# Kernel tuning notes

Hardware: AMD Instinct MI355X
Metric: run time of the kernel (lower is better)

Reference implementation:

```python
import jax, jax.numpy as jnp
import numpy as np


def setup_inputs() -> dict:
    key = jax.random.key(0)
    k1, k2, k3, k4 = jax.random.split(key, 4)
    batch, T, state_dim, action_dim = 64, 1024, 512, 128
    x0 = jax.random.normal(k1, (batch, state_dim), dtype=jnp.float32)
    us = jax.random.normal(k2, (batch, T, action_dim), dtype=jnp.float32)
    # Scale A so the 1024-step linear recurrence stays bounded (spectral radius < 1)
    A = jax.random.normal(k3, (state_dim, state_dim), dtype=jnp.float32) * (0.9 / np.sqrt(state_dim))
    B = jax.random.normal(k4, (action_dim, state_dim), dtype=jnp.float32) * (1.0 / np.sqrt(action_dim))
    return {"x0": x0, "us": us, "A": A, "B": B}


def reference(x0, us, A, B):
    """Linear SSM rollout: x_{t+1} = x_t @ A + u_t @ B, returns xs [batch, T, state_dim]."""
    us_t = jnp.swapaxes(us, 0, 1)  # [T, batch, action_dim]

    def step(x, u):
        x_next = x @ A + u @ B  # [batch, state_dim]
        return x_next, x_next

    _, xs = jax.lax.scan(step, x0, us_t)  # xs: [T, batch, state_dim]
    return jnp.swapaxes(xs, 0, 1)  # [batch, T, state_dim]
```

## Files before the change

### kernel.cpp

```cpp
#include <hip/hip_runtime.h>


typedef __attribute__((ext_vector_type(8))) short bf16x8;
typedef __attribute__((ext_vector_type(8))) unsigned short ushort8;
typedef __attribute__((ext_vector_type(4))) float f32x4;
typedef unsigned short ushort_t;

#define MFMA16(a, b, c) __builtin_amdgcn_mfma_f32_16x16x32_bf16(a, b, c, 0, 0, 0)

#define OFF_AT  0UL
#define OFF_AU  8912896UL
#define OFF_BT  15204352UL
#define OFF_BU  15335424UL
#define OFF_WT  15466496UL
#define OFF_Z   16515072UL
#define OFF_E1S 41680896UL
#define OFF_E2S 50069504UL

__host__ __device__ __forceinline__ int slot_of(int p) {
    if (p == 0) return 16;
    if (p <= 8) return p - 1;
    return 7 + (p >> 3);
}

__device__ __forceinline__ unsigned short f2bf(float f) {
    union { float f; unsigned u; } v; v.f = f;
    unsigned r = v.u + 0x7FFFu + ((v.u >> 16) & 1u);
    return (unsigned short)(r >> 16);
}

__device__ __forceinline__ int sel4(int4 v, int p) {
    return p == 0 ? v.x : p == 1 ? v.y : p == 2 ? v.z : v.w;
}

typedef __attribute__((address_space(3))) unsigned int as3_u32;
typedef __attribute__((address_space(1))) const unsigned int as1_u32;
__device__ __forceinline__ void gll16(const void* g, void* l) {
    __builtin_amdgcn_global_load_lds((as1_u32*)g, (as3_u32*)l, 16, 0, 0);
}

__global__ __launch_bounds__(256) void prep_kernel(const float* __restrict__ x0,
                                                   const float* __restrict__ us,
                                                   const float* __restrict__ A,
                                                   const float* __restrict__ B,
                                                   char* __restrict__ ws) {
    ushort_t* At1 = (ushort_t*)(ws + OFF_AT);
    ushort_t* Au1 = (ushort_t*)(ws + OFF_AU);
    ushort_t* Bt  = (ushort_t*)(ws + OFF_BT);
    ushort_t* Bu  = (ushort_t*)(ws + OFF_BU);
    ushort_t* X0b = (ushort_t*)(ws + OFF_E2S);
    ushort_t* Z   = (ushort_t*)(ws + OFF_Z);
    long idx = (long)blockIdx.x * 256 + threadIdx.x;
    if (idx < 262144) {
        Au1[idx] = f2bf(A[idx]);
    } else if (idx < 524288) {
        long gi = idx - 262144;
        int n = (int)(gi >> 9), k = (int)(gi & 511);
        At1[gi] = f2bf(A[(long)k * 512 + n]);
    } else if (idx < 589824) {
        long i2 = idx - 524288;
        int kp = (int)(i2 >> 9), n = (int)(i2 & 511);
        ushort_t v = f2bf(B[i2]);
        Bt[(long)n * 128 + kp] = v;
        Bu[i2] = v;
    } else if (idx < 593920) {
        long gi = idx - 589824;
        long e0 = gi * 8;
        float4 v0 = *(const float4*)(x0 + e0);
        float4 v1 = *(const float4*)(x0 + e0 + 4);
        ushort8 h = { f2bf(v0.x), f2bf(v0.y), f2bf(v0.z), f2bf(v0.w),
                      f2bf(v1.x), f2bf(v1.y), f2bf(v1.z), f2bf(v1.w) };
        *(ushort8*)(X0b + e0) = h;
    } else if (idx < 1642496) {
        long gi = idx - 593920;
        int row = (int)(gi >> 7), g8 = (int)(gi & 127);
        int c = row >> 6, b = row & 63;
        const float* src = us + (long)b * 131072 + c * 1024 + g8 * 8;
        float4 v0 = *(const float4*)src;
        float4 v1 = *(const float4*)(src + 4);
        ushort8 h = { f2bf(v0.x), f2bf(v0.y), f2bf(v0.z), f2bf(v0.w),
                      f2bf(v1.x), f2bf(v1.y), f2bf(v1.z), f2bf(v1.w) };
        *(ushort8*)(Z + (long)row * 1536 + 512 + g8 * 8) = h;
    } else {
        long gi2 = idx - 1642496;
        if (gi2 < 262144) {
            int n = (int)(gi2 >> 9), k2 = (int)(gi2 & 511);
            At1[(long)16 * 262144 + gi2] = (n == k2) ? (ushort_t)0x3F80 : (ushort_t)0;
        }
    }
}

__global__ __launch_bounds__(256) void pow_stage(char* __restrict__ ws,
                                                 int4 dd, int4 mm, int4 ii, int dual) {
    __shared__ ushort_t ldsX[64 * 512];
    ushort_t* At = (ushort_t*)(ws + OFF_AT);
    ushort_t* Au = (ushort_t*)(ws + OFF_AU);

    int bx = blockIdx.x;
    int nb = bx & 3, mb = (bx >> 2) & 7;
    int prod, pair;
    if (dual) { prod = (bx >> 5) & 1; pair = bx >> 6; }
    else      { prod = 0;             pair = bx >> 5; }
    int d = sel4(dd, pair), m_ = sel4(mm, pair), i_ = sel4(ii, pair);

    const ushort_t *Xp, *Yp; ushort_t* outp;
    if (prod == 0) { Xp = At + (long)slot_of(m_) * 262144; Yp = Au + (long)slot_of(i_) * 262144; outp = At + (long)slot_of(d) * 262144; }
    else           { Xp = Au + (long)slot_of(i_) * 262144; Yp = At + (long)slot_of(m_) * 262144; outp = Au + (long)slot_of(d) * 262144; }

    int tid = threadIdx.x, w = tid >> 6, lane = tid & 63, q = lane >> 4, r = lane & 15;

    for (int i2 = tid; i2 < 64 * 64; i2 += 256) {
        int row = i2 >> 6, c8 = i2 & 63;
        ushort8 v = *(const ushort8*)(Xp + (long)(mb * 64 + row) * 512 + c8 * 8);
        *(ushort8*)&ldsX[row * 512 + ((c8 ^ (row & 7)) << 3)] = v;
    }
    __syncthreads();

    f32x4 acc[4][2];
    for (int a1 = 0; a1 < 4; a1++) for (int b1 = 0; b1 < 2; b1++) acc[a1][b1] = (f32x4){0.f, 0.f, 0.f, 0.f};

    int n0 = nb * 128 + w * 32;
    for (int kt = 0; kt < 16; kt++) {
        bf16x8 b0 = *(const bf16x8*)(Yp + (long)(n0 + r) * 512 + kt * 32 + q * 8);
        bf16x8 b1 = *(const bf16x8*)(Yp + (long)(n0 + 16 + r) * 512 + kt * 32 + q * 8);
        int g2 = kt * 4 + q;
#pragma unroll
        for (int mi = 0; mi < 4; mi++) {
            int row = mi * 16 + r;
            bf16x8 a = *(bf16x8*)&ldsX[row * 512 + ((g2 ^ (row & 7)) << 3)];
            acc[mi][0] = MFMA16(a, b0, acc[mi][0]);
            acc[mi][1] = MFMA16(a, b1, acc[mi][1]);
        }
    }
    for (int mi = 0; mi < 4; mi++) for (int nj = 0; nj < 2; nj++) {
        int m = mb * 64 + mi * 16 + q * 4, n = n0 + nj * 16 + r;
        for (int v = 0; v < 4; v++) outp[(long)(m + v) * 512 + n] = f2bf(acc[mi][nj][v]);
    }
}

__global__ __launch_bounds__(256) void wk_kernel(char* __restrict__ ws) {
    __shared__ ushort_t ldsX[64 * 512];
    ushort_t* At = (ushort_t*)(ws + OFF_AT);
    ushort_t* Bu = (ushort_t*)(ws + OFF_BU);
    ushort_t* Bt = (ushort_t*)(ws + OFF_BT);
    ushort_t* Wt = (ushort_t*)(ws + OFF_WT);

    int bx = blockIdx.x;
    int k8 = bx >> 3, mb = bx & 7;
    int tid = threadIdx.x, w = tid >> 6, lane = tid & 63, q = lane >> 4, r = lane & 15;

    if (k8 == 7) {
        for (int i2 = tid; i2 < 64 * 32; i2 += 256) {
            int row = i2 >> 5, c4 = i2 & 31;
            ushort4 v = *(const ushort4*)(Bt + (long)(mb * 64 + row) * 128 + c4 * 4);
            *(ushort4*)(Wt + (long)(mb * 64 + row) * 128 + c4 * 4) = v;
        }
        return;
    }

    int p = 7 - k8;
    const ushort_t* Xp = At + (long)slot_of(p) * 262144;
    for (int i2 = tid; i2 < 64 * 64; i2 += 256) {
        int row = i2 >> 6, c8 = i2 & 63;
        ushort8 v = *(const ushort8*)(Xp + (long)(mb * 64 + row) * 512 + c8 * 8);
        *(ushort8*)&ldsX[row * 512 + ((c8 ^ (row & 7)) << 3)] = v;
    }
    __syncthreads();

    f32x4 acc[4][2];
    for (int a1 = 0; a1 < 4; a1++) for (int b1 = 0; b1 < 2; b1++) acc[a1][b1] = (f32x4){0.f, 0.f, 0.f, 0.f};

    int n0 = w * 32;
    for (int kt = 0; kt < 16; kt++) {
        bf16x8 b0 = *(const bf16x8*)(Bu + (long)(n0 + r) * 512 + kt * 32 + q * 8);
        bf16x8 b1 = *(const bf16x8*)(Bu + (long)(n0 + 16 + r) * 512 + kt * 32 + q * 8);
        int g2 = kt * 4 + q;
#pragma unroll
        for (int mi = 0; mi < 4; mi++) {
            int row = mi * 16 + r;
            bf16x8 a = *(bf16x8*)&ldsX[row * 512 + ((g2 ^ (row & 7)) << 3)];
            acc[mi][0] = MFMA16(a, b0, acc[mi][0]);
            acc[mi][1] = MFMA16(a, b1, acc[mi][1]);
        }
    }
    ushort_t* Wp = Wt + (long)p * 65536;
    for (int mi = 0; mi < 4; mi++) for (int nj = 0; nj < 2; nj++) {
        int m = mb * 64 + mi * 16 + q * 4, n = n0 + nj * 16 + r;
        for (int v = 0; v < 4; v++) Wp[(long)(m + v) * 128 + n] = f2bf(acc[mi][nj][v]);
    }
}

__global__ __launch_bounds__(256, 4) void e1g(char* __restrict__ ws) {
    __shared__ ushort_t Alds[64 * 64];
    __shared__ ushort_t Blds[128 * 64];
    const ushort_t* Z  = (const ushort_t*)(ws + OFF_Z);
    const ushort_t* Wt = (const ushort_t*)(ws + OFF_WT);
    ushort_t* E1s = (ushort_t*)(ws + OFF_E1S);

    int bx = blockIdx.x;
    int c = bx >> 2, nt = bx & 3;
    int tid = threadIdx.x, w = tid >> 6, lane = tid & 63, q = lane >> 4, r = lane & 15;
    int wr = w >> 1, wc = w & 1;
    int l8 = lane >> 3, srcg = (lane & 7) ^ l8;

    const ushort_t* Xb = Z + (long)c * 64 * 1536 + 512;

    f32x4 acc[2][4];
#pragma unroll
    for (int a1 = 0; a1 < 2; a1++)
#pragma unroll
        for (int b1 = 0; b1 < 4; b1++) acc[a1][b1] = (f32x4){0.f, 0.f, 0.f, 0.f};

    for (int s = 0; s < 16; s++) {
        int k0 = s * 64;
#pragma unroll
        for (int i = 0; i < 2; i++) {
            int row = i * 32 + w * 8 + l8;
            gll16(Xb + (long)row * 1536 + k0 + srcg * 8, &Alds[i * 2048 + w * 512]);
        }
        const ushort_t* Yb = Wt + (long)(7 - (s >> 1)) * 65536 + (s & 1) * 64;
#pragma unroll
        for (int i = 0; i < 4; i++) {
            int row = i * 32 + w * 8 + l8;
            gll16(Yb + (long)(nt * 128 + row) * 128 + srcg * 8, &Blds[i * 2048 + w * 512]);
        }
        __syncthreads();
#pragma unroll
        for (int kt = 0; kt < 2; kt++) {
            int g2 = kt * 4 + q;
            bf16x8 a[2], b[4];
#pragma unroll
            for (int mi = 0; mi < 2; mi++) {
                int row = wr * 32 + mi * 16 + r;
                a[mi] = *(bf16x8*)&Alds[row * 64 + ((g2 ^ (row & 7)) << 3)];
            }
#pragma unroll
            for (int nj = 0; nj < 4; nj++) {
                int row = wc * 64 + nj * 16 + r;
                b[nj] = *(bf16x8*)&Blds[row * 64 + ((g2 ^ (row & 7)) << 3)];
            }
#pragma unroll
            for (int mi = 0; mi < 2; mi++)
#pragma unroll
                for (int nj = 0; nj < 4; nj++)
                    acc[mi][nj] = MFMA16(a[mi], b[nj], acc[mi][nj]);
        }
        __syncthreads();
    }

#pragma unroll
    for (int mi = 0; mi < 2; mi++)
#pragma unroll
        for (int nj = 0; nj < 4; nj++) {
            int m = wr * 32 + mi * 16 + q * 4;
            int n = nt * 128 + wc * 64 + nj * 16 + r;
#pragma unroll
            for (int v = 0; v < 4; v++)
                E1s[(long)c * 32768 + (long)(m + v) * 512 + n] = f2bf(acc[mi][nj][v]);
        }
}

__global__ __launch_bounds__(256, 4) void e2g(char* __restrict__ ws) {
    __shared__ ushort_t Alds[64 * 64];
    __shared__ ushort_t Blds[64 * 64];
    const ushort_t* At  = (const ushort_t*)(ws + OFF_AT);
    const ushort_t* E1s = (const ushort_t*)(ws + OFF_E1S);
    ushort_t* E2s = (ushort_t*)(ws + OFF_E2S);

    int bx = blockIdx.x;
    int g = bx >> 3, ntb = bx & 7;
    int tid = threadIdx.x, w = tid >> 6, lane = tid & 63, q = lane >> 4, r = lane & 15;
    int wr = w >> 1, wc = w & 1;
    int l8 = lane >> 3, srcg = (lane & 7) ^ l8;

    f32x4 acc[2][2];
#pragma unroll
    for (int a1 = 0; a1 < 2; a1++)
#pragma unroll
        for (int b1 = 0; b1 < 2; b1++) acc[a1][b1] = (f32x4){0.f, 0.f, 0.f, 0.f};

    for (int s = 0; s < 64; s++) {
        int t = s >> 3, k0 = (s & 7) * 64;
        const ushort_t* Xp = E1s + (long)(8 * g + t) * 32768;
        const ushort_t* Yb = At + (long)slot_of(8 * (7 - t)) * 262144;
#pragma unroll
        for (int i = 0; i < 2; i++) {
            int row = i * 32 + w * 8 + l8;
            gll16(Xp + (long)row * 512 + k0 + srcg * 8, &Alds[i * 2048 + w * 512]);
            gll16(Yb + (long)(ntb * 64 + row) * 512 + k0 + srcg * 8, &Blds[i * 2048 + w * 512]);
        }
        __syncthreads();
#pragma unroll
        for (int kt = 0; kt < 2; kt++) {
            int g2 = kt * 4 + q;
            bf16x8 a[2], b[2];
#pragma unroll
            for (int mi = 0; mi < 2; mi++) {
                int row = wr * 32 + mi * 16 + r;
                a[mi] = *(bf16x8*)&Alds[row * 64 + ((g2 ^ (row & 7)) << 3)];
            }
#pragma unroll
            for (int nj = 0; nj < 2; nj++) {
                int row = wc * 32 + nj * 16 + r;
                b[nj] = *(bf16x8*)&Blds[row * 64 + ((g2 ^ (row & 7)) << 3)];
            }
#pragma unroll
            for (int mi = 0; mi < 2; mi++)
#pragma unroll
                for (int nj = 0; nj < 2; nj++)
                    acc[mi][nj] = MFMA16(a[mi], b[nj], acc[mi][nj]);
        }
        __syncthreads();
    }

#pragma unroll
    for (int mi = 0; mi < 2; mi++)
#pragma unroll
        for (int nj = 0; nj < 2; nj++) {
            int m = wr * 32 + mi * 16 + q * 4;
            int n = ntb * 64 + wc * 32 + nj * 16 + r;
#pragma unroll
            for (int v = 0; v < 4; v++)
                E2s[(long)(1 + g) * 32768 + (long)(m + v) * 512 + n] = f2bf(acc[mi][nj][v]);
        }
}

__global__ __launch_bounds__(256, 4) void s1x(char* __restrict__ ws) {
    __shared__ ushort_t Alds[64 * 64];
    __shared__ ushort_t Blds[128 * 64];
    const ushort_t* At  = (const ushort_t*)(ws + OFF_AT);
    const ushort_t* E1s = (const ushort_t*)(ws + OFF_E1S);
    const ushort_t* E2s = (const ushort_t*)(ws + OFF_E2S);
    ushort_t* Z = (ushort_t*)(ws + OFF_Z);

    int bx = blockIdx.x;
    int c = bx >> 2, nt = bx & 3;
    int g = c >> 3, j = c & 7;
    int extra = (j == 0 && g >= 1) ? 1 : 0;
    int nterms = 1 + extra + j;
    int S = nterms * 8;
    int tid = threadIdx.x, w = tid >> 6, lane = tid & 63, q = lane >> 4, r = lane & 15;
    int wr = w >> 1, wc = w & 1;
    int l8 = lane >> 3, srcg = (lane & 7) ^ l8;

    auto xptr = [&](int t) -> const ushort_t* {
        if (t == 0) return E2s + (long)g * 32768;
        if (extra && t == 1) return E2s + (long)(g - 1) * 32768;
        return E1s + (long)(8 * g + t - 1 - extra) * 32768;
    };
    auto yptr = [&](int t) -> const ushort_t* {
        int p = (t == 0) ? 8 * j : ((extra && t == 1) ? 64 : 8 * (j - t + extra));
        return At + (long)slot_of(p) * 262144;
    };

    f32x4 acc[2][4];
#pragma unroll
    for (int a1 = 0; a1 < 2; a1++)
#pragma unroll
        for (int b1 = 0; b1 < 4; b1++) acc[a1][b1] = (f32x4){0.f, 0.f, 0.f, 0.f};

    for (int s = 0; s < S; s++) {
        int t = s >> 3, k0 = (s & 7) * 64;
        const ushort_t* Xp = xptr(t);
        const ushort_t* Yb = yptr(t);
#pragma unroll
        for (int i = 0; i < 2; i++) {
            int row = i * 32 + w * 8 + l8;
            gll16(Xp + (long)row * 512 + k0 + srcg * 8, &Alds[i * 2048 + w * 512]);
        }
#pragma unroll
        for (int i = 0; i < 4; i++) {
            int row = i * 32 + w * 8 + l8;
            gll16(Yb + (long)(nt * 128 + row) * 512 + k0 + srcg * 8, &Blds[i * 2048 + w * 512]);
        }
        __syncthreads();
#pragma unroll
        for (int kt = 0; kt < 2; kt++) {
            int g2 = kt * 4 + q;
            bf16x8 a[2], b[4];
#pragma unroll
            for (int mi = 0; mi < 2; mi++) {
                int row = wr * 32 + mi * 16 + r;
                a[mi] = *(bf16x8*)&Alds[row * 64 + ((g2 ^ (row & 7)) << 3)];
            }
#pragma unroll
            for (int nj = 0; nj < 4; nj++) {
                int row = wc * 64 + nj * 16 + r;
                b[nj] = *(bf16x8*)&Blds[row * 64 + ((g2 ^ (row & 7)) << 3)];
            }
#pragma unroll
            for (int mi = 0; mi < 2; mi++)
#pragma unroll
                for (int nj = 0; nj < 4; nj++)
                    acc[mi][nj] = MFMA16(a[mi], b[nj], acc[mi][nj]);
        }
        __syncthreads();
    }

#pragma unroll
    for (int mi = 0; mi < 2; mi++)
#pragma unroll
        for (int nj = 0; nj < 4; nj++) {
            int m = wr * 32 + mi * 16 + q * 4;
            int n = nt * 128 + wc * 64 + nj * 16 + r;
#pragma unroll
            for (int v = 0; v < 4; v++)
                Z[(long)(c * 64 + m + v) * 1536 + n] = f2bf(acc[mi][nj][v]);
        }
}

__global__ __launch_bounds__(256, 4) void outg(float* __restrict__ dout,
                                               char* __restrict__ ws) {
    __shared__ ushort_t Alds[128 * 64];
    __shared__ ushort_t Blds[128 * 64];
    const ushort_t* Z  = (const ushort_t*)(ws + OFF_Z);
    const ushort_t* At = (const ushort_t*)(ws + OFF_AT);
    const ushort_t* Wt = (const ushort_t*)(ws + OFF_WT);

    int bx = blockIdx.x;
    int mt = bx & 63;
    int k  = (bx >> 6) & 7;
    int nt = bx >> 9;
    int tid = threadIdx.x, w = tid >> 6, lane = tid & 63, q = lane >> 4, r = lane & 15;
    int wr = w >> 1, wc = w & 1;
    int l8 = lane >> 3, srcg = (lane & 7) ^ l8;

    const ushort_t* Xb = Z + (long)mt * 128 * 1536;
    const ushort_t* Ya = At + (long)slot_of(k + 1) * 262144;
    int Ks = 8 + 2 * (k + 1);

    f32x4 acc[4][4];
#pragma unroll
    for (int a1 = 0; a1 < 4; a1++)
#pragma unroll
        for (int b1 = 0; b1 < 4; b1++) acc[a1][b1] = (f32x4){0.f, 0.f, 0.f, 0.f};

    for (int s = 0; s < Ks; s++) {
        int k0 = s * 64;
#pragma unroll
        for (int i = 0; i < 4; i++) {
            int row = i * 32 + w * 8 + l8;
            gll16(Xb + (long)row * 1536 + k0 + srcg * 8, &Alds[i * 2048 + w * 512]);
        }
        if (k0 < 512) {
#pragma unroll
            for (int i = 0; i < 4; i++) {
                int row = i * 32 + w * 8 + l8;
                gll16(Ya + (long)(nt * 128 + row) * 512 + k0 + srcg * 8, &Blds[i * 2048 + w * 512]);
            }
        } else {
            int uc = k0 - 512;
            const ushort_t* Yb = Wt + (long)(k - (uc >> 7)) * 65536 + (uc & 127);
#pragma unroll
            for (int i = 0; i < 4; i++) {
                int row = i * 32 + w * 8 + l8;
                gll16(Yb + (long)(nt * 128 + row) * 128 + srcg * 8, &Blds[i * 2048 + w * 512]);
            }
        }
        __syncthreads();
#pragma unroll
        for (int kt = 0; kt < 2; kt++) {
            int g2 = kt * 4 + q;
            bf16x8 a[4], b[4];
#pragma unroll
            for (int mi = 0; mi < 4; mi++) {
                int row = wr * 64 + mi * 16 + r;
                a[mi] = *(bf16x8*)&Alds[row * 64 + ((g2 ^ (row & 7)) << 3)];
            }
#pragma unroll
            for (int nj = 0; nj < 4; nj++) {
                int row = wc * 64 + nj * 16 + r;
                b[nj] = *(bf16x8*)&Blds[row * 64 + ((g2 ^ (row & 7)) << 3)];
            }
#pragma unroll
            for (int mi = 0; mi < 4; mi++)
#pragma unroll
                for (int nj = 0; nj < 4; nj++)
                    acc[mi][nj] = MFMA16(a[mi], b[nj], acc[mi][nj]);
        }
        __syncthreads();
    }

#pragma unroll
    for (int mi = 0; mi < 4; mi++) {
        int m = mt * 128 + wr * 64 + mi * 16 + q * 4;
#pragma unroll
        for (int nj = 0; nj < 4; nj++) {
            int n = nt * 128 + wc * 64 + nj * 16 + r;
#pragma unroll
            for (int v = 0; v < 4; v++) {
                int mm = m + v;
                dout[(long)(mm & 63) * 524288 + (long)(((mm >> 6) << 3) + k) * 512 + n] = acc[mi][nj][v];
            }
        }
    }
}

extern "C" void kernel_launch(void* const* d_in, const int* in_sizes, int n_in,
                              void* d_out, int out_size, void* d_ws, size_t ws_size,
                              hipStream_t stream) {
    const float* x0 = (const float*)d_in[0];
    const float* us = (const float*)d_in[1];
    const float* A  = (const float*)d_in[2];
    const float* B  = (const float*)d_in[3];
    float* dout = (float*)d_out;
    char* ws = (char*)d_ws;

    prep_kernel<<<7440, 256, 0, stream>>>(x0, us, A, B, ws);

    const int stn[6]     = {1, 2, 4, 1, 2, 4};
    const int stdual[6]  = {1, 1, 1, 1, 1, 0};
    const int std_[6][4] = {{2,0,0,0},{3,4,0,0},{5,6,7,8},{16,0,0,0},{24,32,0,0},{40,48,56,64}};
    const int stm[6][4]  = {{1,0,0,0},{2,2,0,0},{4,4,4,4},{8,0,0,0},{16,16,0,0},{32,32,32,32}};
    const int sti[6][4]  = {{1,0,0,0},{1,2,0,0},{1,2,3,4},{8,0,0,0},{8,16,0,0},{8,16,24,32}};
    for (int s = 0; s < 6; s++) {
        int4 dd = {std_[s][0], std_[s][1], std_[s][2], std_[s][3]};
        int4 mm = {stm[s][0], stm[s][1], stm[s][2], stm[s][3]};
        int4 ii = {sti[s][0], sti[s][1], sti[s][2], sti[s][3]};
        int blocks = stn[s] * (stdual[s] ? 64 : 32);
        pow_stage<<<blocks, 256, 0, stream>>>(ws, dd, mm, ii, stdual[s]);
    }

    wk_kernel<<<64, 256, 0, stream>>>(ws);
    e1g<<<512, 256, 0, stream>>>(ws);
    e2g<<<128, 256, 0, stream>>>(ws);
    s1x<<<512, 256, 0, stream>>>(ws);
    outg<<<2048, 256, 0, stream>>>(dout, ws);
}
```

Baseline: 280.4 us.

## Fold wk kernel into pow stage 3 and reorder s1x blocks for balance

```diff
diff --git a/kernel.cpp b/kernel.cpp
--- a/kernel.cpp
+++ b/kernel.cpp
@@ -90,19 +90,11 @@
     }
 }
 
-__global__ __launch_bounds__(256) void pow_stage(char* __restrict__ ws,
-                                                 int4 dd, int4 mm, int4 ii, int dual) {
-    __shared__ ushort_t ldsX[64 * 512];
+__device__ __forceinline__ void pow_tile(char* __restrict__ ws, ushort_t* ldsX,
+                                         int d, int m_, int i_, int prod,
+                                         int mb, int nb) {
     ushort_t* At = (ushort_t*)(ws + OFF_AT);
     ushort_t* Au = (ushort_t*)(ws + OFF_AU);
-
-    int bx = blockIdx.x;
-    int nb = bx & 3, mb = (bx >> 2) & 7;
-    int prod, pair;
-    if (dual) { prod = (bx >> 5) & 1; pair = bx >> 6; }
-    else      { prod = 0;             pair = bx >> 5; }
-    int d = sel4(dd, pair), m_ = sel4(mm, pair), i_ = sel4(ii, pair);
-
     const ushort_t *Xp, *Yp; ushort_t* outp;
     if (prod == 0) { Xp = At + (long)slot_of(m_) * 262144; Yp = Au + (long)slot_of(i_) * 262144; outp = At + (long)slot_of(d) * 262144; }
     else           { Xp = Au + (long)slot_of(i_) * 262144; Yp = At + (long)slot_of(m_) * 262144; outp = Au + (long)slot_of(d) * 262144; }
@@ -138,15 +130,13 @@
     }
 }
 
-__global__ __launch_bounds__(256) void wk_kernel(char* __restrict__ ws) {
-    __shared__ ushort_t ldsX[64 * 512];
+__device__ __forceinline__ void wk_tile(char* __restrict__ ws, ushort_t* ldsX,
+                                        int k8, int mb) {
     ushort_t* At = (ushort_t*)(ws + OFF_AT);
     ushort_t* Bu = (ushort_t*)(ws + OFF_BU);
     ushort_t* Bt = (ushort_t*)(ws + OFF_BT);
     ushort_t* Wt = (ushort_t*)(ws + OFF_WT);
 
-    int bx = blockIdx.x;
-    int k8 = bx >> 3, mb = bx & 7;
     int tid = threadIdx.x, w = tid >> 6, lane = tid & 63, q = lane >> 4, r = lane & 15;
 
     if (k8 == 7) {
@@ -188,6 +178,26 @@
         int m = mb * 64 + mi * 16 + q * 4, n = n0 + nj * 16 + r;
         for (int v = 0; v < 4; v++) Wp[(long)(m + v) * 128 + n] = f2bf(acc[mi][nj][v]);
     }
+}
+
+__global__ __launch_bounds__(256) void pow_stage(char* __restrict__ ws,
+                                                 int4 dd, int4 mm, int4 ii,
+                                                 int dual, int wkbase) {
+    __shared__ ushort_t ldsX[64 * 512];
+    int bx = blockIdx.x;
+
+    if (wkbase > 0 && bx >= wkbase) {
+        int widx = bx - wkbase;
+        wk_tile(ws, ldsX, widx >> 3, widx & 7);
+        return;
+    }
+
+    int nb = bx & 3, mb = (bx >> 2) & 7;
+    int prod, pair;
+    if (dual) { prod = (bx >> 5) & 1; pair = bx >> 6; }
+    else      { prod = 0;             pair = bx >> 5; }
+    int d = sel4(dd, pair), m_ = sel4(mm, pair), i_ = sel4(ii, pair);
+    pow_tile(ws, ldsX, d, m_, i_, prod, mb, nb);
 }
 
 __global__ __launch_bounds__(256, 4) void e1g(char* __restrict__ ws) {
@@ -334,8 +344,10 @@
     ushort_t* Z = (ushort_t*)(ws + OFF_Z);
 
     int bx = blockIdx.x;
-    int c = bx >> 2, nt = bx & 3;
-    int g = c >> 3, j = c & 7;
+    int t0 = bx >> 2, nt = bx & 3;
+    int g = t0 >> 3, jj = t0 & 7;
+    int j = (g >= 8) ? (7 - jj) : jj;
+    int c = g * 8 + j;
     int extra = (j == 0 && g >= 1) ? 1 : 0;
     int nterms = 1 + extra + j;
     int S = nterms * 8;
@@ -510,6 +522,7 @@
 
     const int stn[6]     = {1, 2, 4, 1, 2, 4};
     const int stdual[6]  = {1, 1, 1, 1, 1, 0};
+    const int stwk[6]    = {0, 0, 0, 64, 0, 0};
     const int std_[6][4] = {{2,0,0,0},{3,4,0,0},{5,6,7,8},{16,0,0,0},{24,32,0,0},{40,48,56,64}};
     const int stm[6][4]  = {{1,0,0,0},{2,2,0,0},{4,4,4,4},{8,0,0,0},{16,16,0,0},{32,32,32,32}};
     const int sti[6][4]  = {{1,0,0,0},{1,2,0,0},{1,2,3,4},{8,0,0,0},{8,16,0,0},{8,16,24,32}};
@@ -517,11 +530,10 @@
         int4 dd = {std_[s][0], std_[s][1], std_[s][2], std_[s][3]};
         int4 mm = {stm[s][0], stm[s][1], stm[s][2], stm[s][3]};
         int4 ii = {sti[s][0], sti[s][1], sti[s][2], sti[s][3]};
-        int blocks = stn[s] * (stdual[s] ? 64 : 32);
-        pow_stage<<<blocks, 256, 0, stream>>>(ws, dd, mm, ii, stdual[s]);
-    }
-
-    wk_kernel<<<64, 256, 0, stream>>>(ws);
+        int blocks = stn[s] * (stdual[s] ? 64 : 32) + (stwk[s] ? 64 : 0);
+        pow_stage<<<blocks, 256, 0, stream>>>(ws, dd, mm, ii, stdual[s], stwk[s]);
+    }
+
     e1g<<<512, 256, 0, stream>>>(ws);
     e2g<<<128, 256, 0, stream>>>(ws);
     s1x<<<512, 256, 0, stream>>>(ws);
```

New measurement: 270.3 us. 3.6% less time.
